# Performance work log

Measured on AMD Instinct MI355X. Metric: run time of the kernel, lower is better.

The kernel has to match this reference:

```python
import jax, jax.numpy as jnp
import numpy as np

NG, K, LEN_KEEP = 128, 32, 32  # n_groups, group_size, int(128*(1-0.75))
ENC_HEADS, DEC_HEADS = 12, 16


def _fps(xyz, init, npoint):
    # iterative farthest point sampling; xyz (B,N,3), init (B,) start indices
    B, N, _ = xyz.shape
    def step(carry, _):
        dmin, far = carry
        c = jnp.take_along_axis(xyz, far[:, None, None], axis=1)  # (B,1,3)
        dmin = jnp.minimum(dmin, jnp.sum((xyz - c) ** 2, -1))
        return (dmin, jnp.argmax(dmin, -1)), far
    _, cents = jax.lax.scan(step, (jnp.full((B, N), 1e10, xyz.dtype), init), None, length=npoint)
    return cents.T  # (B, npoint)


def _knn(xyz, cents, k):
    # squared-distance knn (same ordering as euclidean cdist + topk smallest)
    x2 = jnp.sum(xyz * xyz, -1)          # (B,N)
    c2 = jnp.sum(cents * cents, -1)      # (B,M)
    d = c2[:, :, None] + x2[:, None, :] - 2.0 * jnp.einsum('bmc,bnc->bmn', cents, xyz)
    idx = jax.lax.top_k(-d, k)[1]        # (B,M,k)
    return jax.vmap(lambda p, i: p[i])(xyz, idx)  # (B,M,k,3)


def _bn(x, g, b):
    # train-mode BatchNorm1d over (batch, spatial), channel-last x (BM,k,C)
    m = x.mean((0, 1))
    v = x.var((0, 1))
    return (x - m) * jax.lax.rsqrt(v + 1e-5) * g + b


def _ln(x, g, b):
    m = x.mean(-1, keepdims=True)
    v = ((x - m) ** 2).mean(-1, keepdims=True)
    return (x - m) * jax.lax.rsqrt(v + 1e-5) * g + b


def _layer(x, qw, qb, ow, ob, l1g, l1b, f1w, f1b, f2w, f2b, l2g, l2b, nh):
    # post-norm TransformerEncoderLayer (relu FFN, no dropout = eval mode)
    B, S, D = x.shape
    dh = D // nh
    q, k, v = jnp.split(x @ qw.T + qb, 3, axis=-1)
    q = q.reshape(B, S, nh, dh); k = k.reshape(B, S, nh, dh); v = v.reshape(B, S, nh, dh)
    att = jax.nn.softmax(jnp.einsum('bqhd,bkhd->bhqk', q, k) * (1.0 / float(np.sqrt(dh))), axis=-1)
    o = jnp.einsum('bhqk,bkhd->bqhd', att, v).reshape(B, S, D) @ ow.T + ob
    x = _ln(x + o, l1g, l1b)
    f = jax.nn.relu(x @ f1w.T + f1b) @ f2w.T + f2b
    return _ln(x + f, l2g, l2b)


def _stack(x, qw, qb, ow, ob, l1g, l1b, f1w, f1b, f2w, f2b, l2g, l2b, nh):
    for i in range(qw.shape[0]):
        x = _layer(x, qw[i], qb[i], ow[i], ob[i], l1g[i], l1b[i], f1w[i], f1b[i], f2w[i], f2b[i], l2g[i], l2b[i], nh)
    return x


def _forward(xyz, fps_init, ids_shuffle, cw1, cb1, g1, be1, cw2, cb2, g2, be2, cw3, cb3, g3, be3, pos_w, pos_b, eqw, eqb, eow, eob, el1g, el1b, ef1w, ef1b, ef2w, ef2b, el2g, el2b, dew, deb, mtok, dpw, dpb, dqw, dqb, dow, dob, dl1g, dl1b, df1w, df1b, df2w, df2b, dl2g, dl2b, prw, prb):
    B = xyz.shape[0]
    cent_idx = _fps(xyz, fps_init, NG)
    cxyz = jax.vmap(lambda p, i: p[i])(xyz, cent_idx)      # (B,NG,3)
    gn = _knn(xyz, cxyz, K) - cxyz[:, :, None, :]          # (B,NG,K,3) centered groups
    h = gn.reshape(-1, K, 3)
    h = jax.nn.relu(_bn(h @ cw1.T + cb1, g1, be1))
    h = jax.nn.relu(_bn(h @ cw2.T + cb2, g2, be2))
    h = _bn(h @ cw3.T + cb3, g3, be3)
    tokens = h.max(axis=1).reshape(B, NG, -1)              # (B,NG,768)
    x = tokens + cxyz @ pos_w.T + pos_b
    ids_restore = jnp.argsort(ids_shuffle, axis=1)
    xk = jnp.take_along_axis(x, ids_shuffle[:, :LEN_KEEP, None], axis=1)
    mask = jnp.ones((B, NG), xyz.dtype).at[:, :LEN_KEEP].set(0.0)
    mask = jnp.take_along_axis(mask, ids_restore, axis=1)
    lat = _stack(xk, eqw, eqb, eow, eob, el1g, el1b, ef1w, ef1b, ef2w, ef2b, el2g, el2b, ENC_HEADS)
    y = lat @ dew.T + deb
    mt = jnp.broadcast_to(mtok, (B, NG - LEN_KEEP, mtok.shape[0]))
    y_ = jnp.take_along_axis(jnp.concatenate([y, mt], axis=1), ids_restore[:, :, None], axis=1)
    yd = y_ + cxyz @ dpw.T + dpb
    dec = _stack(yd, dqw, dqb, dow, dob, dl1g, dl1b, df1w, df1b, df2w, df2b, dl2g, dl2b, DEC_HEADS)
    pred = dec @ prw.T + prb                               # (B,NG,K*3)
    target = gn.reshape(B, NG, -1)                         # same FPS seed -> same centroids in loss branch
    l = ((pred - target) ** 2).mean(-1)
    loss = (l * mask).sum() / mask.sum()
    return loss, pred, mask


def setup_inputs():
    ks = iter(jax.random.split(jax.random.key(0), 64))
    def W(*shape):
        return jax.random.normal(next(ks), shape, jnp.float32) * 0.02
    B, N, D, DD, Le, Ld = 32, 8192, 768, 512, 12, 8
    d = {}
    d['xyz'] = jax.random.normal(next(ks), (B, N, 3), jnp.float32)
    d['fps_init'] = jax.random.randint(next(ks), (B,), 0, N)
    d['ids_shuffle'] = jnp.argsort(jax.random.uniform(next(ks), (B, NG)), axis=1)
    d['cw1'], d['cb1'], d['g1'], d['be1'] = W(64, 3), jnp.zeros(64), jnp.ones(64), jnp.zeros(64)
    d['cw2'], d['cb2'], d['g2'], d['be2'] = W(128, 64), jnp.zeros(128), jnp.ones(128), jnp.zeros(128)
    d['cw3'], d['cb3'], d['g3'], d['be3'] = W(D, 128), jnp.zeros(D), jnp.ones(D), jnp.zeros(D)
    d['pos_w'], d['pos_b'] = W(D, 3), jnp.zeros(D)
    d['eqw'], d['eqb'] = W(Le, 3 * D, D), jnp.zeros((Le, 3 * D))
    d['eow'], d['eob'] = W(Le, D, D), jnp.zeros((Le, D))
    d['el1g'], d['el1b'] = jnp.ones((Le, D)), jnp.zeros((Le, D))
    d['ef1w'], d['ef1b'] = W(Le, 4 * D, D), jnp.zeros((Le, 4 * D))
    d['ef2w'], d['ef2b'] = W(Le, D, 4 * D), jnp.zeros((Le, D))
    d['el2g'], d['el2b'] = jnp.ones((Le, D)), jnp.zeros((Le, D))
    d['dew'], d['deb'] = W(DD, D), jnp.zeros(DD)
    d['mtok'] = jnp.zeros(DD)
    d['dpw'], d['dpb'] = W(DD, 3), jnp.zeros(DD)
    d['dqw'], d['dqb'] = W(Ld, 3 * DD, DD), jnp.zeros((Ld, 3 * DD))
    d['dow'], d['dob'] = W(Ld, DD, DD), jnp.zeros((Ld, DD))
    d['dl1g'], d['dl1b'] = jnp.ones((Ld, DD)), jnp.zeros((Ld, DD))
    d['df1w'], d['df1b'] = W(Ld, 4 * DD, DD), jnp.zeros((Ld, 4 * DD))
    d['df2w'], d['df2b'] = W(Ld, DD, 4 * DD), jnp.zeros((Ld, DD))
    d['dl2g'], d['dl2b'] = jnp.ones((Ld, DD)), jnp.zeros((Ld, DD))
    d['prw'], d['prb'] = W(K * 3, DD), jnp.zeros(K * 3)
    return d


def reference(xyz, fps_init, ids_shuffle, cw1, cb1, g1, be1, cw2, cb2, g2, be2, cw3, cb3, g3, be3, pos_w, pos_b, eqw, eqb, eow, eob, el1g, el1b, ef1w, ef1b, ef2w, ef2b, el2g, el2b, dew, deb, mtok, dpw, dpb, dqw, dqb, dow, dob, dl1g, dl1b, df1w, df1b, df2w, df2b, dl2g, dl2b, prw, prb):
    return _forward(xyz, fps_init, ids_shuffle, cw1, cb1, g1, be1, cw2, cb2, g2, be2, cw3, cb3, g3, be3, pos_w, pos_b, eqw, eqb, eow, eob, el1g, el1b, ef1w, ef1b, ef2w, ef2b, el2g, el2b, dew, deb, mtok, dpw, dpb, dqw, dqb, dow, dob, dl1g, dl1b, df1w, df1b, df2w, df2b, dl2g, dl2b, prw, prb)
```

## Files before the change

### kernel.cpp

```cpp
#include <hip/hip_runtime.h>
#include <cmath>

#define BB 32
#define NPTS 8192
#define NG 128
#define KNB 32
#define LK 32
#define DE 768
#define DD 512
#define NLE 12
#define NLD 8

typedef __bf16 bf16x8 __attribute__((ext_vector_type(8)));
typedef float  f32x4  __attribute__((ext_vector_type(4)));
typedef unsigned long long u64;

#define WAITV(N) asm volatile("s_waitcnt vmcnt(" #N ")" ::: "memory")

static __device__ __forceinline__ bf16x8 pack8(float4 a, float4 b) {
    bf16x8 h;
    h[0] = (__bf16)a.x; h[1] = (__bf16)a.y; h[2] = (__bf16)a.z; h[3] = (__bf16)a.w;
    h[4] = (__bf16)b.x; h[5] = (__bf16)b.y; h[6] = (__bf16)b.z; h[7] = (__bf16)b.w;
    return h;
}
// ... 41 lines not shown
        float best = -1.0f; int bi = 0;
        #pragma unroll
        for (int k = 0; k < 16; ++k) {
            int n = tid + (k << 9);
            float dx = x[k] - cx, dy = y[k] - cy, dz = z[k] - cz;
            float d = dx * dx + dy * dy + dz * dz;
            float dm = dmin[k];
            if (d < dm) dm = d;
            dmin[k] = dm;
            if (dm > best) { best = dm; bi = n; }
        }
        u64 key = ((u64)__float_as_uint(best) << 32) | (unsigned)(8191 - bi);
        #pragma unroll
        for (int d = 32; d >= 1; d >>= 1) {
            u64 k2 = __shfl_down(key, d);
            if (k2 > key) key = k2;
        }
        if ((tid & 63) == 0) red[t & 1][tid >> 6] = key;
        __syncthreads();
        u64 kb = red[t & 1][0];
        #pragma unroll
        for (int w = 1; w < 8; ++w) {
            u64 k2 = red[t & 1][w];
            if (k2 > kb) kb = k2;
        }
        far = 8191 - (int)(kb & 0xFFFFFFFFu);
    }
}

__global__ __launch_bounds__(256) void knn_kernel(
    const float* __restrict__ xyz, const float* __restrict__ cxyz,
    float* __restrict__ gn)
{
#pragma clang fp contract(off)
    const int bm = blockIdx.x;
    const int b = bm / NG;
    const float* P = xyz + (size_t)b * NPTS * 3;
    __shared__ u64 cand[512];
    __shared__ u64 tmins[4];
    __shared__ int wcnt[4];
    __shared__ int order[KNB];
    const int tid = threadIdx.x;
    const int wv = tid >> 6, lane = tid & 63;
    const float cx = cxyz[bm * 3 + 0], cy = cxyz[bm * 3 + 1], cz = cxyz[bm * 3 + 2];
    const float c2 = cx * cx + cy * cy + cz * cz;
    unsigned fk[32];
    float bestf = 1e31f; int bi = 1 << 30;
    #pragma unroll
    for (int j = 0; j < 32; ++j) {
        int n = tid + (j << 8);
        float x = P[n * 3 + 0], y = P[n * 3 + 1], z = P[n * 3 + 2];
        float x2 = x * x + y * y + z * z;
        float dt = cx * x + cy * y + cz * z;
        float v = (c2 + x2) - 2.0f * dt;
        fk[j] = fkey(v);
        if (v < bestf) { bestf = v; bi = n; }
    }
    u64 mk = ((u64)fkey(bestf) << 32) | (unsigned)bi;
    {
        u64 v = mk;
        #pragma unroll
        for (int k = 2; k <= 64; k <<= 1) {
            #pragma unroll
            for (int j = k >> 1; j > 0; j >>= 1) {
                u64 o = __shfl_xor(v, j);
                bool up = ((lane & k) == 0);
                bool lower = ((lane & j) == 0);
                u64 mn = (v < o) ? v : o;
                u64 mx = (v < o) ? o : v;
                v = (up == lower) ? mn : mx;
            }
        }
        u64 Tw = __shfl(v, 31);
        if (lane == 0) tmins[wv] = Tw;
    }
    __syncthreads();
    u64 T = tmins[0];
    #pragma unroll
    for (int w = 1; w < 4; ++w) { u64 k2 = tmins[w]; if (k2 < T) T = k2; }
    int c = 0;
    #pragma unroll
    for (int j = 0; j < 32; ++j) {
        u64 key = ((u64)fk[j] << 32) | (unsigned)(tid + (j << 8));
        c += (key <= T) ? 1 : 0;
    }
    int s = c;
    #pragma unroll
    for (int d = 1; d < 64; d <<= 1) {
        int t2 = __shfl_up(s, d);
        if (lane >= d) s += t2;
    }
    int excl = s - c;
    if (lane == 63) wcnt[wv] = s;
    __syncthreads();
    int base = 0;
    for (int w = 0; w < wv; ++w) base += wcnt[w];
    int etot = wcnt[0] + wcnt[1] + wcnt[2] + wcnt[3];

    if (etot <= 512) {
        int pos = base + excl;
        #pragma unroll
        for (int j = 0; j < 32; ++j) {
            u64 key = ((u64)fk[j] << 32) | (unsigned)(tid + (j << 8));
            if (key <= T) cand[pos++] = key;
        }
        __syncthreads();
        for (int si = tid; si < etot; si += 256) {
            u64 my = cand[si];
            int r = 0;
            for (int j2 = 0; j2 < etot; ++j2) r += (cand[j2] < my) ? 1 : 0;
            if (r < KNB) order[r] = (int)(my & 0xFFFFFFFFu);
        }
        __syncthreads();
    } else {
        u64 bk = ~0ull;
        #pragma unroll
        for (int j = 0; j < 32; ++j) {
            u64 key = ((u64)fk[j] << 32) | (unsigned)(tid + (j << 8));
            if (key < bk) bk = key;
        }
        for (int r = 0; r < KNB; ++r) {
            u64 kk = bk;
            #pragma unroll
            for (int dd = 32; dd >= 1; dd >>= 1) {
                u64 k2 = __shfl_down(kk, dd);
                if (k2 < kk) kk = k2;
            }
            if (lane == 0) cand[(r & 1) * 4 + wv] = kk;
            __syncthreads();
            u64 kb = cand[(r & 1) * 4 + 0];
            #pragma unroll
            for (int w = 1; w < 4; ++w) { u64 k2 = cand[(r & 1) * 4 + w]; if (k2 < kb) kb = k2; }
            if (tid == 0) order[r] = (int)(kb & 0xFFFFFFFFu);
            if ((int)(kb & 255u) == tid) {
                int sj = (int)((kb & 0xFFFFFFFFu) >> 8);
                #pragma unroll
                for (int j = 0; j < 32; ++j) if (j == sj) fk[j] = 0xFFFFFFFFu;
                bk = ~0ull;
                #pragma unroll
                for (int j = 0; j < 32; ++j) {
                    u64 key = ((u64)fk[j] << 32) | (unsigned)(tid + (j << 8));
                    if (key < bk) bk = key;
                }
            }
            __syncthreads();
        }
    }
    if (tid < KNB) {
        int n = order[tid];
        gn[((size_t)bm * KNB + tid) * 3 + 0] = P[n * 3 + 0] - cx;
        gn[((size_t)bm * KNB + tid) * 3 + 1] = P[n * 3 + 1] - cy;
        gn[((size_t)bm * KNB + tid) * 3 + 2] = P[n * 3 + 2] - cz;
    }
}

__global__ void cvt_bf16_kernel(const float* __restrict__ src, __bf16* __restrict__ dst, int n8)
{
    int i = blockIdx.x * 256 + threadIdx.x;
    if (i >= n8) return;
    const float4* p = (const float4*)(src + (size_t)i * 8);
    *(bf16x8*)(dst + (size_t)i * 8) = pack8(p[0], p[1]);
}

struct CvtTab {
    const float* src[10];
    __bf16* dst[10];
    int cum[11];
};
__global__ void cvt_multi_kernel(CvtTab t)
{
    int i = blockIdx.x * 256 + threadIdx.x;
    if (i >= t.cum[10]) return;
    int seg = 0;
    #pragma unroll
    for (int k = 1; k < 10; ++k) seg += (i >= t.cum[k]) ? 1 : 0;
    int local = i - t.cum[seg];
    const float4* p = (const float4*)(t.src[seg] + (size_t)local * 8);
    *(bf16x8*)(t.dst[seg] + (size_t)local * 8) = pack8(p[0], p[1]);
}

__global__ void embed1_kernel(const float* __restrict__ gn, const float* __restrict__ w,
                              const float* __restrict__ bias, float* __restrict__ h1)
{
    int i = blockIdx.x * 256 + threadIdx.x;
    if (i >= 131072 * 64) return;
    int r = i >> 6, c = i & 63;
    const float* p = gn + (size_t)r * 3;
    h1[i] = p[0] * w[c * 3 + 0] + p[1] * w[c * 3 + 1] + p[2] * w[c * 3 + 2] + bias[c];
}

template <int C>
__global__ __launch_bounds__(256) void colstats_kernel(const float* __restrict__ X,
                                                       double* __restrict__ st, int Mrows)
{
    constexpr int RL = 256 / C;
    const int c = threadIdx.x % C;
    const int rl = threadIdx.x / C;
    double s = 0.0, s2 = 0.0;
    int rows_per_block = (Mrows + gridDim.x - 1) / gridDim.x;
    int r0 = blockIdx.x * rows_per_block;
    int r1 = min(r0 + rows_per_block, Mrows);
    for (int r = r0 + rl; r < r1; r += RL) {
        float v = X[(size_t)r * C + c];
        s += v; s2 += (double)v * v;
    }
    __shared__ double sh[2][256];
    sh[0][threadIdx.x] = s; sh[1][threadIdx.x] = s2;
    __syncthreads();
    if (rl == 0) {
        for (int j = 1; j < RL; ++j) { s += sh[0][j * C + c]; s2 += sh[1][j * C + c]; }
        atomicAdd(&st[c], s);
        atomicAdd(&st[C + c], s2);
    }
}

__global__ void bn_finalize(const double* __restrict__ st, const float* __restrict__ g,
                            const float* __restrict__ be, float* __restrict__ sc,
                            float* __restrict__ shb, int C)
{
    int c = blockIdx.x * 64 + threadIdx.x;
    if (c >= C) return;
    double m = st[c] / 131072.0;
    double var = st[C + c] / 131072.0 - m * m;
    if (var < 0.0) var = 0.0;
    float rs = rsqrtf((float)var + 1e-5f);
    sc[c] = rs * g[c];
    shb[c] = be[c] - (float)m * rs * g[c];
}

__global__ void bn_apply_bf16(const float* __restrict__ x, const float* __restrict__ sc,
                              const float* __restrict__ shb, __bf16* __restrict__ y,
                              int total, int C)
{
    int i = blockIdx.x * 256 + threadIdx.x;
    if (i >= total) return;
    int c = i % C;
    float v = x[i] * sc[c] + shb[c];
    v = fmaxf(v, 0.0f);
    y[i] = (__bf16)v;
}

template <int BM, int WM, int WN, int DEPTH>
__global__ __launch_bounds__(256) void gemm_bf16(
    const __bf16* __restrict__ A, const __bf16* __restrict__ W,
    const float* __restrict__ bias, float* __restrict__ Cf, __bf16* __restrict__ Cb,
    int M, int N, int K, int Kc, int relu)
{
    constexpr int MR = BM / WM / 16;
    constexpr int NR = 128 / WN / 16;
    constexpr int CA = BM * 8 / 256;
    __shared__ __bf16 As[DEPTH][BM * 64];
    __shared__ __bf16 Ws[DEPTH][128 * 64];
    const int tid = threadIdx.x;
    const int lane = tid & 63;
    const int wave = tid >> 6;
    const int wm = wave / WN, wn = wave % WN;
    const int m0 = blockIdx.y * BM, n0 = blockIdx.x * 128;
    const int kb = blockIdx.z * Kc;

    f32x4 acc[MR][NR] = {};

    auto stage = [&](int buf, int kt) {
        #pragma unroll
        for (int j = 0; j < CA; ++j) {
            int cb = j * 256 + (wave << 6);
            int c  = cb + lane;
            int row = c >> 3;
            int kcs = (c & 7) ^ (row & 7);
            gload16(A + (size_t)(m0 + row) * K + kb + kt + kcs * 8, &As[buf][cb * 8]);
        }
        #pragma unroll
        for (int j = 0; j < 4; ++j) {
            int cb = j * 256 + (wave << 6);
            int c  = cb + lane;
            int row = c >> 3;
            int kcs = (c & 7) ^ (row & 7);
            gload16(W + (size_t)(n0 + row) * K + kb + kt + kcs * 8, &Ws[buf][cb * 8]);
        }
    };
    auto compute = [&](int buf) {
        #pragma unroll
        for (int ks = 0; ks < 2; ++ks) {
            bf16x8 af[MR], bfr[NR];
            int kc = ks * 4 + (lane >> 4);
            #pragma unroll
            for (int i = 0; i < MR; ++i) {
                int rowA = wm * (BM / WM) + i * 16 + (lane & 15);
                af[i] = *(bf16x8*)&As[buf][rowA * 64 + ((kc ^ (rowA & 7)) * 8)];
            }
            #pragma unroll
            for (int j = 0; j < NR; ++j) {
                int rowB = wn * (128 / WN) + j * 16 + (lane & 15);
                bfr[j] = *(bf16x8*)&Ws[buf][rowB * 64 + ((kc ^ (rowB & 7)) * 8)];
            }
            #pragma unroll
            for (int i = 0; i < MR; ++i)
                #pragma unroll
                for (int j = 0; j < NR; ++j)
                    acc[i][j] = __builtin_amdgcn_mfma_f32_16x16x32_bf16(af[i], bfr[j], acc[i][j], 0, 0, 0);
        }
    };

    const int nt = Kc >> 6;
    if constexpr (DEPTH == 3) {
        stage(0, 0);
        if (nt > 1) stage(1, 64);
        for (int t = 0; t < nt; ++t) {
            if (t < nt - 1) { if constexpr (BM == 64) WAITV(6); else WAITV(8); }
            else            WAITV(0);
            __syncthreads();
            if (t + 2 < nt) stage((t + 2) % 3, (t + 2) << 6);
            compute(t % 3);
        }
    } else {
        stage(0, 0);
        if (nt > 1) stage(1, 64);
        for (int t = 0; t < nt; ++t) {
            if (t < nt - 1) { if constexpr (BM == 64) WAITV(6); else WAITV(8); }
            else            WAITV(0);
            __syncthreads();
            compute(t % 2);
            if (t + 2 <= nt - 1) {
                __syncthreads();
                stage(t % 2, (t + 2) << 6);
            }
        }
    }

    float* Co = Cf ? Cf + (size_t)blockIdx.z * M * N : nullptr;
    #pragma unroll
    for (int j = 0; j < NR; ++j) {
        int col = n0 + wn * (128 / WN) + j * 16 + (lane & 15);
        if (col >= N) continue;
        float bv = (blockIdx.z == 0) ? bias[col] : 0.0f;
        #pragma unroll
        for (int i = 0; i < MR; ++i) {
            #pragma unroll
            for (int r = 0; r < 4; ++r) {
                int rowm = m0 + wm * (BM / WM) + i * 16 + (lane >> 4) * 4 + r;
                float v = acc[i][j][r] + bv;
                if (relu) v = fmaxf(v, 0.0f);
                if (Co) Co[(size_t)rowm * N + col] = v;
                if (Cb) Cb[(size_t)rowm * N + col] = (__bf16)v;
            }
        }
    }
}

__global__ __launch_bounds__(256) void embed3_mfma(
    const __bf16* __restrict__ A, const __bf16* __restrict__ W,
    const float* __restrict__ cb3,
    float* __restrict__ gmax, float* __restrict__ gmin, double* __restrict__ st3)
{
    __shared__ __bf16 As[2][128 * 64];
    __shared__ __bf16 Ws[2][128 * 64];
    const int tid = threadIdx.x;
    const int lane = tid & 63;
    const int wave = tid >> 6;
    const int wm = wave >> 1, wn = wave & 1;
    const int m0 = blockIdx.y * 128, n0 = blockIdx.x * 128;
    const int K = 128;

    f32x4 acc[4][4] = {};

    auto stage = [&](int buf, int kt) {
        #pragma unroll
        for (int j = 0; j < 4; ++j) {
            int cb = j * 256 + (wave << 6);
            int c  = cb + lane;
            int row = c >> 3;
            int kcs = (c & 7) ^ (row & 7);
            gload16(A + (size_t)(m0 + row) * K + kt + kcs * 8, &As[buf][cb * 8]);
            gload16(W + (size_t)(n0 + row) * K + kt + kcs * 8, &Ws[buf][cb * 8]);
        }
    };
    auto compute = [&](int buf) {
        #pragma unroll
        for (int ks = 0; ks < 2; ++ks) {
            bf16x8 af[4], bfr[4];
            int kc = ks * 4 + (lane >> 4);
            #pragma unroll
            for (int i = 0; i < 4; ++i) {
                int rowA = wm * 64 + i * 16 + (lane & 15);
                af[i] = *(bf16x8*)&As[buf][rowA * 64 + ((kc ^ (rowA & 7)) * 8)];
                int rowB = wn * 64 + i * 16 + (lane & 15);
                bfr[i] = *(bf16x8*)&Ws[buf][rowB * 64 + ((kc ^ (rowB & 7)) * 8)];
            }
            #pragma unroll
            for (int i = 0; i < 4; ++i)
                #pragma unroll
                for (int j = 0; j < 4; ++j)
                    acc[i][j] = __builtin_amdgcn_mfma_f32_16x16x32_bf16(af[i], bfr[j], acc[i][j], 0, 0, 0);
        }
    };

    stage(0, 0);
    stage(1, 64);
    WAITV(8);
    __syncthreads();
    compute(0);
    WAITV(0);
    __syncthreads();
    compute(1);

    #pragma unroll
    for (int j = 0; j < 4; ++j) {
        int col = n0 + wn * 64 + j * 16 + (lane & 15);
        float bv = cb3[col];
        float stot = 0.0f, s2tot = 0.0f;
        #pragma unroll
        for (int gi = 0; gi < 2; ++gi) {
            float mx = -1e30f, mn = 1e30f, s = 0.0f, s2 = 0.0f;
            #pragma unroll
            for (int ii = 0; ii < 2; ++ii) {
                f32x4 a = acc[gi * 2 + ii][j];
                #pragma unroll
                for (int r = 0; r < 4; ++r) {
                    float v = a[r] + bv;
                    mx = fmaxf(mx, v); mn = fminf(mn, v);
                    s += v; s2 += v * v;
                }
            }
            #pragma unroll
            for (int d = 16; d < 64; d <<= 1) {
                mx = fmaxf(mx, __shfl_xor(mx, d));
                mn = fminf(mn, __shfl_xor(mn, d));
                s  += __shfl_xor(s, d);
                s2 += __shfl_xor(s2, d);
            }
            stot += s; s2tot += s2;
            if (lane < 16) {
                int g = (m0 >> 5) + wm * 2 + gi;
                gmax[(size_t)g * 768 + col] = mx;
                gmin[(size_t)g * 768 + col] = mn;
            }
        }
        if (lane < 16) {
            double* stp = st3 + (size_t)(blockIdx.y & 31) * 1536;
            atomicAdd(&stp[col], (double)stot);
            atomicAdd(&stp[768 + col], (double)s2tot);
        }
    }
}

__global__ void bn3_finalize(const double* __restrict__ st3, const float* __restrict__ g,
                             const float* __restrict__ be, float* __restrict__ a3,
                             float* __restrict__ c3)
{
    int c = blockIdx.x * 256 + threadIdx.x;
    if (c >= 768) return;
    double s = 0.0, s2 = 0.0;
    for (int p = 0; p < 32; ++p) { s += st3[(size_t)p * 1536 + c]; s2 += st3[(size_t)p * 1536 + 768 + c]; }
    double m = s / 131072.0;
    double var = s2 / 131072.0 - m * m;
    if (var < 0.0) var = 0.0;
    float rs = rsqrtf((float)var + 1e-5f);
    a3[c] = rs * g[c];
    c3[c] = be[c] - (float)m * rs * g[c];
}

__global__ void tokens_pos(const float* __restrict__ gmax, const float* __restrict__ gmin,
                           const float* __restrict__ a3, const float* __restrict__ c3,
                           const float* __restrict__ cxyz, const float* __restrict__ posw,
                           const float* __restrict__ posb, float* __restrict__ x)
{
    int i = blockIdx.x * 256 + threadIdx.x;
    if (i >= 4096 * 768) return;
    int c = i % 768, g = i / 768;
    float a = a3[c];
    float tok = (a >= 0.0f ? a * gmax[i] : a * gmin[i]) + c3[c];
    float px = cxyz[g * 3 + 0], py = cxyz[g * 3 + 1], pz = cxyz[g * 3 + 2];
    x[i] = tok + px * posw[c * 3 + 0] + py * posw[c * 3 + 1] + pz * posw[c * 3 + 2] + posb[c];
}

__global__ void restore_kernel(const int* __restrict__ shuffle, int* __restrict__ restore,
                               float* __restrict__ maskv)
{
    int j = blockIdx.x * 256 + threadIdx.x;
    if (j >= BB * NG) return;
    int b = j / NG, p = j % NG;
    int dst = b * NG + shuffle[j];
    restore[dst] = p;
    maskv[dst] = (p < LK) ? 0.0f : 1.0f;
}

__global__ void gather_xk(const float* __restrict__ xfull, const int* __restrict__ shuffle,
                          float* __restrict__ xe, __bf16* __restrict__ xeb)
{
    int i = blockIdx.x * 256 + threadIdx.x;
    if (i >= BB * LK * DE) return;
    int c = i % DE;
    int s = (i / DE) % LK;
    int b = i / (DE * LK);
    float v = xfull[((size_t)b * NG + shuffle[b * NG + s]) * DE + c];
    xe[i] = v;
    xeb[i] = (__bf16)v;
}

__global__ void yd_build(const float* __restrict__ ykp, const int* __restrict__ restore,
                         const float* __restrict__ mtok, const float* __restrict__ cxyz,
                         const float* __restrict__ dpw, const float* __restrict__ dpb,
                         float* __restrict__ xd, __bf16* __restrict__ xdb)
{
    const size_t PS = (size_t)1024 * DD;
    int i = blockIdx.x * 256 + threadIdx.x;
    if (i >= BB * NG * DD) return;
    int c = i % DD;
    int g = i / DD;
    int b = g / NG;
    int r = restore[g];
    float base;
    if (r < LK) {
        size_t o = (size_t)(b * LK + r) * DD + c;
        base = ykp[o] + ykp[PS + o] + ykp[2 * PS + o] + ykp[3 * PS + o];
    } else {
        base = mtok[c];
    }
    float px = cxyz[g * 3 + 0], py = cxyz[g * 3 + 1], pz = cxyz[g * 3 + 2];
    float v = base + px * dpw[c * 3 + 0] + py * dpw[c * 3 + 1] + pz * dpw[c * 3 + 2] + dpb[c];
    xd[i] = v;
    xdb[i] = (__bf16)v;
}

template <int S, int DH, int NH>
__global__ __launch_bounds__(256) void dattn_kernel(const float* __restrict__ qkv,
                                                    __bf16* __restrict__ o, float scale)
{
    constexpr int D = NH * DH;
    constexpr int SQ = DH + 8;
    constexpr int SV = S + 8;
    __shared__ __bf16 Qb[S * SQ];
    __shared__ __bf16 Kb[S * SQ];
    __shared__ __bf16 Vt[DH * SV];
    __shared__ __bf16 Pb[S * SV];
    const int h = blockIdx.x % NH;
    const int b = blockIdx.x / NH;
    const int tid = threadIdx.x;
    const int lane = tid & 63, wv = tid >> 6;
    const float* base = qkv + (size_t)b * S * 3 * D + h * DH;
    for (int i = tid; i < S * (DH / 4); i += 256) {
        int s = i / (DH / 4), c4 = (i % (DH / 4)) * 4;
        const float* rp = base + (size_t)s * 3 * D;
        float4 q = *(const float4*)(rp + c4);
        float4 k = *(const float4*)(rp + D + c4);
        float4 v = *(const float4*)(rp + 2 * D + c4);
        __bf16 q4[4] = {(__bf16)q.x, (__bf16)q.y, (__bf16)q.z, (__bf16)q.w};
        __bf16 k4[4] = {(__bf16)k.x, (__bf16)k.y, (__bf16)k.z, (__bf16)k.w};
        *(ushort4*)&Qb[s * SQ + c4] = *(ushort4*)q4;
        *(ushort4*)&Kb[s * SQ + c4] = *(ushort4*)k4;
        Vt[(c4 + 0) * SV + s] = (__bf16)v.x;
        Vt[(c4 + 1) * SV + s] = (__bf16)v.y;
        Vt[(c4 + 2) * SV + s] = (__bf16)v.z;
        Vt[(c4 + 3) * SV + s] = (__bf16)v.w;
    }
    __syncthreads();
    const int q0 = wv * 32;
    const int arow = lane & 15;
    const int kch = (lane >> 4) * 8;
    const int rrow = (lane >> 4) * 4;
    f32x4 sc[2][8];
    {
        bf16x8 af0 = *(bf16x8*)&Qb[(q0 + arow) * SQ + kch];
        bf16x8 af1 = *(bf16x8*)&Qb[(q0 + 16 + arow) * SQ + kch];
        f32x4 z = {0.0f, 0.0f, 0.0f, 0.0f};
        #pragma unroll
        for (int j = 0; j < 8; ++j) {
            bf16x8 bf_ = *(bf16x8*)&Kb[(j * 16 + arow) * SQ + kch];
            sc[0][j] = __builtin_amdgcn_mfma_f32_16x16x32_bf16(af0, bf_, z, 0, 0, 0);
            sc[1][j] = __builtin_amdgcn_mfma_f32_16x16x32_bf16(af1, bf_, z, 0, 0, 0);
        }
    }
    #pragma unroll
    for (int i = 0; i < 2; ++i) {
        #pragma unroll
        for (int r = 0; r < 4; ++r) {
            float m = -1e30f;
            #pragma unroll
            for (int j = 0; j < 8; ++j) m = fmaxf(m, sc[i][j][r]);
            #pragma unroll
            for (int d = 8; d >= 1; d >>= 1) m = fmaxf(m, __shfl_xor(m, d));
            float sum = 0.0f;
            #pragma unroll
            for (int j = 0; j < 8; ++j) {
                float e = expf((sc[i][j][r] - m) * scale);
                sc[i][j][r] = e;
                sum += e;
            }
            #pragma unroll
            for (int d = 8; d >= 1; d >>= 1) sum += __shfl_xor(sum, d);
            float inv = 1.0f / sum;
            int row = q0 + i * 16 + rrow + r;
            #pragma unroll
            for (int j = 0; j < 8; ++j)
                Pb[row * SV + j * 16 + (lane & 15)] = (__bf16)(sc[i][j][r] * inv);
        }
    }
    #pragma unroll
    for (int i = 0; i < 2; ++i) {
        #pragma unroll
        for (int j2 = 0; j2 < 2; ++j2) {
            f32x4 a2 = {0.0f, 0.0f, 0.0f, 0.0f};
            #pragma unroll
            for (int ks = 0; ks < 4; ++ks) {
                bf16x8 pa = *(bf16x8*)&Pb[(q0 + i * 16 + arow) * SV + ks * 32 + kch];
                bf16x8 vb = *(bf16x8*)&Vt[(j2 * 16 + arow) * SV + ks * 32 + kch];
                a2 = __builtin_amdgcn_mfma_f32_16x16x32_bf16(pa, vb, a2, 0, 0, 0);
            }
            #pragma unroll
            for (int r = 0; r < 4; ++r) {
                int q = q0 + i * 16 + rrow + r;
                o[((size_t)(b * S + q)) * D + h * DH + j2 * 16 + (lane & 15)] = (__bf16)a2[r];
            }
        }
    }
}

template <int S, int DH, int NH>
__global__ __launch_bounds__(64) void eattn_kernel(const float* __restrict__ qkv,
                                                   __bf16* __restrict__ o, float scale)
{
    constexpr int D = NH * DH;
    constexpr int SQ = DH + 8;
    constexpr int SV = S + 8;
    __shared__ __bf16 Qb[S * SQ];
    __shared__ __bf16 Kb[S * SQ];
    __shared__ __bf16 Vt[DH * SV];
    __shared__ __bf16 Pb[S * SV];
    const int h = blockIdx.x % NH;
    const int b = blockIdx.x / NH;
    const int lane = threadIdx.x;
    const float* base = qkv + (size_t)b * S * 3 * D + h * DH;
    for (int i = lane; i < S * (DH / 4); i += 64) {
        int s = i / (DH / 4), c4 = (i % (DH / 4)) * 4;
        const float* rp = base + (size_t)s * 3 * D;
        float4 q = *(const float4*)(rp + c4);
        float4 k = *(const float4*)(rp + D + c4);
        float4 v = *(const float4*)(rp + 2 * D + c4);
        __bf16 q4[4] = {(__bf16)q.x, (__bf16)q.y, (__bf16)q.z, (__bf16)q.w};
        __bf16 k4[4] = {(__bf16)k.x, (__bf16)k.y, (__bf16)k.z, (__bf16)k.w};
        *(ushort4*)&Qb[s * SQ + c4] = *(ushort4*)q4;
        *(ushort4*)&Kb[s * SQ + c4] = *(ushort4*)k4;
        Vt[(c4 + 0) * SV + s] = (__bf16)v.x;
        Vt[(c4 + 1) * SV + s] = (__bf16)v.y;
        Vt[(c4 + 2) * SV + s] = (__bf16)v.z;
        Vt[(c4 + 3) * SV + s] = (__bf16)v.w;
    }
    __syncthreads();
    const int arow = lane & 15;
    const int kch = (lane >> 4) * 8;
    const int rrow = (lane >> 4) * 4;
    f32x4 sc[2][2] = {};
    #pragma unroll
    for (int ks = 0; ks < 2; ++ks) {
        bf16x8 af0 = *(bf16x8*)&Qb[(arow) * SQ + ks * 32 + kch];
        bf16x8 af1 = *(bf16x8*)&Qb[(16 + arow) * SQ + ks * 32 + kch];
        #pragma unroll
        for (int j = 0; j < 2; ++j) {
            bf16x8 bf_ = *(bf16x8*)&Kb[(j * 16 + arow) * SQ + ks * 32 + kch];
            sc[0][j] = __builtin_amdgcn_mfma_f32_16x16x32_bf16(af0, bf_, sc[0][j], 0, 0, 0);
            sc[1][j] = __builtin_amdgcn_mfma_f32_16x16x32_bf16(af1, bf_, sc[1][j], 0, 0, 0);
        }
    }
    #pragma unroll
    for (int i = 0; i < 2; ++i) {
        #pragma unroll
        for (int r = 0; r < 4; ++r) {
            float m = fmaxf(sc[i][0][r], sc[i][1][r]);
            #pragma unroll
            for (int d = 8; d >= 1; d >>= 1) m = fmaxf(m, __shfl_xor(m, d));
            float sum = 0.0f;
            #pragma unroll
            for (int j = 0; j < 2; ++j) {
                float e = expf((sc[i][j][r] - m) * scale);
                sc[i][j][r] = e;
                sum += e;
            }
            #pragma unroll
            for (int d = 8; d >= 1; d >>= 1) sum += __shfl_xor(sum, d);
            float inv = 1.0f / sum;
            int row = i * 16 + rrow + r;
            #pragma unroll
            for (int j = 0; j < 2; ++j)
                Pb[row * SV + j * 16 + (lane & 15)] = (__bf16)(sc[i][j][r] * inv);
        }
    }
    __syncthreads();
    #pragma unroll
    for (int i = 0; i < 2; ++i) {
        bf16x8 pa = *(bf16x8*)&Pb[(i * 16 + arow) * SV + kch];
        #pragma unroll
        for (int j2 = 0; j2 < 4; ++j2) {
            bf16x8 vb = *(bf16x8*)&Vt[(j2 * 16 + arow) * SV + kch];
            f32x4 z = {0.0f, 0.0f, 0.0f, 0.0f};
            f32x4 a2 = __builtin_amdgcn_mfma_f32_16x16x32_bf16(pa, vb, z, 0, 0, 0);
            #pragma unroll
            for (int r = 0; r < 4; ++r) {
                int q = i * 16 + rrow + r;
                o[((size_t)(b * S + q)) * D + h * DH + j2 * 16 + (lane & 15)] = (__bf16)a2[r];
            }
        }
    }
}

template <int D, int SK>
__global__ __launch_bounds__(256) void ln_res(float* __restrict__ x, const float* __restrict__ part,
                                              size_t pstride,
                                              const float* __restrict__ g, const float* __restrict__ b,
                                              __bf16* __restrict__ xb)
{
    constexpr int J = D / 256;
    __shared__ float pr[2][4];
    const size_t off = (size_t)blockIdx.x * D;
    const int tid = threadIdx.x;
    float vals[J];
    float s = 0.0f, s2 = 0.0f;
    #pragma unroll
    for (int j = 0; j < J; ++j) {
        int i = tid + j * 256;
        float v = x[off + i];
        #pragma unroll
        for (int sk = 0; sk < SK; ++sk) v += part[(size_t)sk * pstride + off + i];
        vals[j] = v; s += v; s2 += v * v;
    }
    #pragma unroll
    for (int d = 32; d >= 1; d >>= 1) { s += __shfl_down(s, d); s2 += __shfl_down(s2, d); }
    if ((tid & 63) == 0) { pr[0][tid >> 6] = s; pr[1][tid >> 6] = s2; }
    __syncthreads();
    float st = pr[0][0] + pr[0][1] + pr[0][2] + pr[0][3];
    float s2t = pr[1][0] + pr[1][1] + pr[1][2] + pr[1][3];
    float m = st / D;
    float var = s2t / D - m * m;
    if (var < 0.0f) var = 0.0f;
    float rs = rsqrtf(var + 1e-5f);
    #pragma unroll
    for (int j = 0; j < J; ++j) {
        int i = tid + j * 256;
        float v = (vals[j] - m) * rs * g[i] + b[i];
        x[off + i] = v;
        xb[off + i] = (__bf16)v;
    }
}

__global__ __launch_bounds__(128) void loss_l(const float* __restrict__ pred,
                                              const float* __restrict__ target,
                                              const float* __restrict__ maskv,
                                              float* __restrict__ lm)
{
    const int g = blockIdx.x;
    __shared__ float red[128];
    int t = threadIdx.x;
    float s = 0.0f;
    if (t < 96) {
        float d = pred[(size_t)g * 96 + t] - target[(size_t)g * 96 + t];
        s = d * d;
    }
    red[t] = s; __syncthreads();
    for (int st = 64; st > 0; st >>= 1) { if (t < st) red[t] += red[t + st]; __syncthreads(); }
    if (t == 0) lm[g] = (red[0] / 96.0f) * maskv[g];
}

__global__ __launch_bounds__(1024) void loss_final(const float* __restrict__ lm,
                                                   const float* __restrict__ maskv,
                                                   float* __restrict__ out)
{
    __shared__ float r1[1024], r2[1024];
    int t = threadIdx.x;
    float a = 0.0f, b = 0.0f;
    for (int i = t; i < BB * NG; i += 1024) { a += lm[i]; b += maskv[i]; }
    r1[t] = a; r2[t] = b; __syncthreads();
    for (int st = 512; st > 0; st >>= 1) { if (t < st) { r1[t] += r1[t + st]; r2[t] += r2[t + st]; } __syncthreads(); }
    if (t == 0) out[0] = r1[0] / r2[0];
}

extern "C" void kernel_launch(void* const* d_in, const int* in_sizes, int n_in,
                              void* d_out, int out_size, void* d_ws, size_t ws_size,
                              hipStream_t stream)
{
    (void)in_sizes; (void)n_in; (void)out_size; (void)ws_size;
    const float* xyz        = (const float*)d_in[0];
    const int*   fps_init   = (const int*)d_in[1];
    const int*   ids_shuf   = (const int*)d_in[2];
    const float* cw1 = (const float*)d_in[3];  const float* cb1 = (const float*)d_in[4];
    const float* g1  = (const float*)d_in[5];  const float* be1 = (const float*)d_in[6];
    const float* cw2 = (const float*)d_in[7];  const float* cb2 = (const float*)d_in[8];
    const float* g2  = (const float*)d_in[9];  const float* be2 = (const float*)d_in[10];
    const float* cw3 = (const float*)d_in[11]; const float* cb3 = (const float*)d_in[12];
    const float* g3  = (const float*)d_in[13]; const float* be3 = (const float*)d_in[14];
    const float* posw = (const float*)d_in[15]; const float* posb = (const float*)d_in[16];
    const float* eqw = (const float*)d_in[17]; const float* eqb = (const float*)d_in[18];
    const float* eow = (const float*)d_in[19]; const float* eob = (const float*)d_in[20];
    const float* el1g = (const float*)d_in[21]; const float* el1b = (const float*)d_in[22];
    const float* ef1w = (const float*)d_in[23]; const float* ef1b = (const float*)d_in[24];
    const float* ef2w = (const float*)d_in[25]; const float* ef2b = (const float*)d_in[26];
    const float* el2g = (const float*)d_in[27]; const float* el2b = (const float*)d_in[28];
    const float* dew = (const float*)d_in[29]; const float* deb = (const float*)d_in[30];
    const float* mtok = (const float*)d_in[31];
    const float* dpw = (const float*)d_in[32]; const float* dpb = (const float*)d_in[33];
    const float* dqw = (const float*)d_in[34]; const float* dqb = (const float*)d_in[35];
    const float* dow = (const float*)d_in[36]; const float* dob = (const float*)d_in[37];
    const float* dl1g = (const float*)d_in[38]; const float* dl1b = (const float*)d_in[39];
    const float* df1w = (const float*)d_in[40]; const float* df1b = (const float*)d_in[41];
    const float* df2w = (const float*)d_in[42]; const float* df2b = (const float*)d_in[43];
    const float* dl2g = (const float*)d_in[44]; const float* dl2b = (const float*)d_in[45];
    const float* prw = (const float*)d_in[46]; const float* prb = (const float*)d_in[47];
    float* out = (float*)d_out;
    float* pred = out + 1;
    float* maskv = out + 1 + (size_t)BB * NG * KNB * 3;

    char* ws = (char*)d_ws;
    size_t off = 0;
    auto alloc = [&](size_t bytes) -> void* {
        void* p = ws + off;
        off = (off + bytes + 255) & ~(size_t)255;
        return p;
    };
    double* st1 = (double*)alloc(128 * 8);
    double* st2 = (double*)alloc(256 * 8);
    double* st3 = (double*)alloc((size_t)32 * 1536 * 8);
    float* sc1 = (float*)alloc(64 * 4);  float* sh1 = (float*)alloc(64 * 4);
    float* sc2 = (float*)alloc(128 * 4); float* sh2 = (float*)alloc(128 * 4);
    float* a3 = (float*)alloc(768 * 4);  float* c3 = (float*)alloc(768 * 4);
    int* restore = (int*)alloc(4096 * 4);
    float* cxyz = (float*)alloc(12288 * 4);
    float* gn   = (float*)alloc((size_t)393216 * 4);
    __bf16* cw2b = (__bf16*)alloc((size_t)128 * 64 * 2);
    __bf16* cw3b = (__bf16*)alloc((size_t)768 * 128 * 2);
    float* xfull = (float*)alloc((size_t)4096 * 768 * 4);
    float* xe    = (float*)alloc((size_t)1024 * 768 * 4);
    __bf16* xeb  = (__bf16*)alloc((size_t)1024 * 768 * 2);
    float* qkve  = (float*)alloc((size_t)1024 * 2304 * 4);
    __bf16* oeb  = (__bf16*)alloc((size_t)1024 * 768 * 2);
    __bf16* fe1b = (__bf16*)alloc((size_t)1024 * 3072 * 2);
    float* xd    = (float*)alloc((size_t)4096 * 512 * 4);
    __bf16* xdb  = (__bf16*)alloc((size_t)4096 * 512 * 2);
    float* qkvd  = (float*)alloc((size_t)4096 * 1536 * 4);
    __bf16* odb  = (__bf16*)alloc((size_t)4096 * 512 * 2);
    __bf16* fd1b = (__bf16*)alloc((size_t)4096 * 2048 * 2);
    float* lm    = (float*)alloc(4096 * 4);

    __bf16* eqwb  = (__bf16*)alloc((size_t)NLE * 3 * DE * DE * 2);
    __bf16* eowb  = (__bf16*)alloc((size_t)NLE * DE * DE * 2);
    __bf16* ef1wb = (__bf16*)alloc((size_t)NLE * 4 * DE * DE * 2);
    __bf16* ef2wb = (__bf16*)alloc((size_t)NLE * 4 * DE * DE * 2);
    __bf16* dewb  = (__bf16*)alloc((size_t)DD * DE * 2);
    __bf16* dqwb  = (__bf16*)alloc((size_t)NLD * 3 * DD * DD * 2);
    __bf16* dowb  = (__bf16*)alloc((size_t)NLD * DD * DD * 2);
    __bf16* df1wb = (__bf16*)alloc((size_t)NLD * 4 * DD * DD * 2);
    __bf16* df2wb = (__bf16*)alloc((size_t)NLD * 4 * DD * DD * 2);
    __bf16* prwb  = (__bf16*)alloc((size_t)128 * 512 * 2);

    char* U = (char*)eqwb;
    float*  h1   = (float*)U;
    __bf16* h1b  = (__bf16*)(U + (size_t)33554432);
    float*  h2   = (float*)(U + (size_t)50331648);
    __bf16* h2b  = (__bf16*)(U + (size_t)117440512);
    float*  gmax = (float*)(U + (size_t)150994944);
    float*  gmin = (float*)(U + (size_t)163577856);

    size_t stats_bytes = (size_t)((char*)st3 + (size_t)32 * 1536 * 8 - (char*)st1);
    hipMemsetAsync((void*)st1, 0, stats_bytes, stream);

    auto cvt = [&](const float* src, __bf16* dst, size_t n) {
        int n8 = (int)(n / 8);
        cvt_bf16_kernel<<<(n8 + 255) / 256, 256, 0, stream>>>(src, dst, n8);
    };
    auto gemm = [&](const __bf16* A, const __bf16* Wt, const float* bias,
                    float* Cf, __bf16* Cb, int M, int N, int K, int relu) {
        int nb128 = ((N + 127) / 128) * (M / 128);
        if (nb128 < 256) {
            dim3 grid((N + 127) / 128, M / 64, 1);
            gemm_bf16<64, 1, 4, 3><<<grid, 256, 0, stream>>>(A, Wt, bias, Cf, Cb, M, N, K, K, relu);
        } else {
            dim3 grid((N + 127) / 128, M / 128, 1);
            gemm_bf16<128, 2, 2, 2><<<grid, 256, 0, stream>>>(A, Wt, bias, Cf, Cb, M, N, K, K, relu);
        }
    };
    auto gemmSK = [&](const __bf16* A, const __bf16* Wt, const float* bias,
                      float* Cf, int M, int N, int K, int SK) {
        dim3 grid((N + 127) / 128, M / 64, SK);
        gemm_bf16<64, 1, 4, 3><<<grid, 256, 0, stream>>>(A, Wt, bias, Cf, nullptr, M, N, K, K / SK, 0);
    };

    cvt(cw2, cw2b, 128 * 64);
    cvt(cw3, cw3b, 768 * 128);

    fps_kernel<<<BB, 512, 0, stream>>>(xyz, fps_init, cxyz);
    knn_kernel<<<BB * NG, 256, 0, stream>>>(xyz, cxyz, gn);

    embed1_kernel<<<(131072 * 64 + 255) / 256, 256, 0, stream>>>(gn, cw1, cb1, h1);
    colstats_kernel<64><<<256, 256, 0, stream>>>(h1, st1, 131072);
    bn_finalize<<<1, 64, 0, stream>>>(st1, g1, be1, sc1, sh1, 64);
    bn_apply_bf16<<<(131072 * 64 + 255) / 256, 256, 0, stream>>>(h1, sc1, sh1, h1b, 131072 * 64, 64);
    gemm(h1b, cw2b, cb2, h2, nullptr, 131072, 128, 64, 0);
    colstats_kernel<128><<<256, 256, 0, stream>>>(h2, st2, 131072);
    bn_finalize<<<2, 64, 0, stream>>>(st2, g2, be2, sc2, sh2, 128);
    bn_apply_bf16<<<(131072 * 128 + 255) / 256, 256, 0, stream>>>(h2, sc2, sh2, h2b, 131072 * 128, 128);
    embed3_mfma<<<dim3(6, 1024), 256, 0, stream>>>(h2b, cw3b, cb3, gmax, gmin, st3);
    bn3_finalize<<<3, 256, 0, stream>>>(st3, g3, be3, a3, c3);
    tokens_pos<<<(4096 * 768 + 255) / 256, 256, 0, stream>>>(gmax, gmin, a3, c3, cxyz, posw, posb, xfull);

    restore_kernel<<<16, 256, 0, stream>>>(ids_shuf, restore, maskv);
    gather_xk<<<(BB * LK * DE + 255) / 256, 256, 0, stream>>>(xfull, ids_shuf, xe, xeb);

    {
        CvtTab t;
        const float* srcs[10] = {eqw, eow, ef1w, ef2w, dew, dqw, dow, df1w, df2w, prw};
        __bf16* dsts[10] = {eqwb, eowb, ef1wb, ef2wb, dewb, dqwb, dowb, df1wb, df2wb, prwb};
        size_t ns[10] = {
            (size_t)NLE * 3 * DE * DE, (size_t)NLE * DE * DE,
            (size_t)NLE * 4 * DE * DE, (size_t)NLE * 4 * DE * DE,
            (size_t)DD * DE,
            (size_t)NLD * 3 * DD * DD, (size_t)NLD * DD * DD,
            (size_t)NLD * 4 * DD * DD, (size_t)NLD * 4 * DD * DD,
            (size_t)96 * 512
        };
        int cum = 0;
        t.cum[0] = 0;
        for (int k = 0; k < 10; ++k) {
            t.src[k] = srcs[k]; t.dst[k] = dsts[k];
            cum += (int)(ns[k] / 8);
            t.cum[k + 1] = cum;
        }
        cvt_multi_kernel<<<(cum + 255) / 256, 256, 0, stream>>>(t);
        hipMemsetAsync((void*)(prwb + (size_t)96 * 512), 0, (size_t)32 * 512 * 2, stream);
    }

    const size_t PSE = (size_t)1024 * DE;
    const size_t PSD = (size_t)4096 * DD;

    for (int l = 0; l < NLE; ++l) {
        gemm(xeb, eqwb + (size_t)l * 3 * DE * DE, eqb + (size_t)l * 3 * DE, qkve, nullptr, 1024, 3 * DE, DE, 0);
        eattn_kernel<LK, 64, 12><<<BB * 12, 64, 0, stream>>>(qkve, oeb, 0.125f);
        gemmSK(oeb, eowb + (size_t)l * DE * DE, eob + (size_t)l * DE, xfull, 1024, DE, DE, 4);
        ln_res<DE, 4><<<BB * LK, 256, 0, stream>>>(xe, xfull, PSE, el1g + (size_t)l * DE, el1b + (size_t)l * DE, xeb);
        gemm(xeb, ef1wb + (size_t)l * 4 * DE * DE, ef1b + (size_t)l * 4 * DE, nullptr, fe1b, 1024, 4 * DE, DE, 1);
        gemmSK(fe1b, ef2wb + (size_t)l * DE * 4 * DE, ef2b + (size_t)l * DE, xfull, 1024, DE, 4 * DE, 4);
        ln_res<DE, 4><<<BB * LK, 256, 0, stream>>>(xe, xfull, PSE, el2g + (size_t)l * DE, el2b + (size_t)l * DE, xeb);
    }

    gemmSK(xeb, dewb, deb, qkve, 1024, DD, DE, 4);
    yd_build<<<(BB * NG * DD + 255) / 256, 256, 0, stream>>>(qkve, restore, mtok, cxyz, dpw, dpb, xd, xdb);

    const float dsc = (float)(1.0 / sqrt(32.0));
    for (int l = 0; l < NLD; ++l) {
        gemm(xdb, dqwb + (size_t)l * 3 * DD * DD, dqb + (size_t)l * 3 * DD, qkvd, nullptr, 4096, 3 * DD, DD, 0);
        dattn_kernel<NG, 32, 16><<<BB * 16, 256, 0, stream>>>(qkvd, odb, dsc);
        gemmSK(odb, dowb + (size_t)l * DD * DD, dob + (size_t)l * DD, qkvd, 4096, DD, DD, 2);
        ln_res<DD, 2><<<BB * NG, 256, 0, stream>>>(xd, qkvd, PSD, dl1g + (size_t)l * DD, dl1b + (size_t)l * DD, xdb);
        gemm(xdb, df1wb + (size_t)l * 4 * DD * DD, df1b + (size_t)l * 4 * DD, nullptr, fd1b, 4096, 4 * DD, DD, 1);
        gemmSK(fd1b, df2wb + (size_t)l * DD * 4 * DD, df2b + (size_t)l * DD, qkvd, 4096, DD, 4 * DD, 2);
        ln_res<DD, 2><<<BB * NG, 256, 0, stream>>>(xd, qkvd, PSD, dl2g + (size_t)l * DD, dl2b + (size_t)l * DD, xdb);
    }

    gemm(xdb, prwb, prb, pred, nullptr, 4096, 96, 512, 0);
    loss_l<<<BB * NG, 128, 0, stream>>>(pred, gn, maskv, lm);
    loss_final<<<1, 1024, 0, stream>>>(lm, maskv, out);
}
```

Before: 2.419 ms.

## Store QKV in bf16, fuse token gather into tokens_pos, split-K prediction head

The QKV projections now write bf16 instead of fp32, and both attention kernels load bf16x8 vectors directly, which halves QKV traffic and drops the in-kernel conversion. tokens_pos now writes only the kept tokens straight into the encoder input via the restore map, which removes the full xfull write and the separate gather kernel. The final projection uses split-K with the partial sums reduced inside loss_l. The GEMM pipeline loop is unified across depths, and gmax/gmin/predp reuse existing buffers. Risks are reduced precision in QKV and aliasing errors if the reused buffers are still live when overwritten.

```diff
diff --git a/kernel.cpp b/kernel.cpp
--- a/kernel.cpp
+++ b/kernel.cpp
@@ -367,29 +367,15 @@
     };
 
     const int nt = Kc >> 6;
-    if constexpr (DEPTH == 3) {
-        stage(0, 0);
-        if (nt > 1) stage(1, 64);
-        for (int t = 0; t < nt; ++t) {
-            if (t < nt - 1) { if constexpr (BM == 64) WAITV(6); else WAITV(8); }
-            else            WAITV(0);
-            __syncthreads();
-            if (t + 2 < nt) stage((t + 2) % 3, (t + 2) << 6);
-            compute(t % 3);
-        }
-    } else {
-        stage(0, 0);
-        if (nt > 1) stage(1, 64);
-        for (int t = 0; t < nt; ++t) {
-            if (t < nt - 1) { if constexpr (BM == 64) WAITV(6); else WAITV(8); }
-            else            WAITV(0);
-            __syncthreads();
-            compute(t % 2);
-            if (t + 2 <= nt - 1) {
-                __syncthreads();
-                stage(t % 2, (t + 2) << 6);
-            }
-        }
+    stage(0, 0);
+    if (DEPTH > 2 && nt > 1) stage(1, 64);
+    for (int t = 0; t < nt; ++t) {
+        int ahead = min(nt - 1, t + DEPTH - 2) - t;
+        if (ahead >= 1) { if constexpr (BM == 64) WAITV(6); else WAITV(8); }
+        else            WAITV(0);
+        __syncthreads();
+        if (t + DEPTH - 1 < nt) stage((t + DEPTH - 1) % DEPTH, (t + DEPTH - 1) << 6);
+        compute(t % DEPTH);
     }
 
     float* Co = Cf ? Cf + (size_t)blockIdx.z * M * N : nullptr;
@@ -527,15 +513,22 @@
 __global__ void tokens_pos(const float* __restrict__ gmax, const float* __restrict__ gmin,
                            const float* __restrict__ a3, const float* __restrict__ c3,
                            const float* __restrict__ cxyz, const float* __restrict__ posw,
-                           const float* __restrict__ posb, float* __restrict__ x)
+                           const float* __restrict__ posb, const int* __restrict__ restore,
+                           float* __restrict__ xe, __bf16* __restrict__ xeb)
 {
     int i = blockIdx.x * 256 + threadIdx.x;
     if (i >= 4096 * 768) return;
     int c = i % 768, g = i / 768;
+    int r = restore[g];
+    if (r >= LK) return;
     float a = a3[c];
     float tok = (a >= 0.0f ? a * gmax[i] : a * gmin[i]) + c3[c];
     float px = cxyz[g * 3 + 0], py = cxyz[g * 3 + 1], pz = cxyz[g * 3 + 2];
-    x[i] = tok + px * posw[c * 3 + 0] + py * posw[c * 3 + 1] + pz * posw[c * 3 + 2] + posb[c];
+    float v = tok + px * posw[c * 3 + 0] + py * posw[c * 3 + 1] + pz * posw[c * 3 + 2] + posb[c];
+    int b = g >> 7;
+    size_t idx = ((size_t)(b * LK + r)) * DE + c;
+    xe[idx] = v;
+    xeb[idx] = (__bf16)v;
 }
 
 __global__ void restore_kernel(const int* __restrict__ shuffle, int* __restrict__ restore,
@@ -547,19 +540,6 @@
     int dst = b * NG + shuffle[j];
     restore[dst] = p;
     maskv[dst] = (p < LK) ? 0.0f : 1.0f;
-}
-
-__global__ void gather_xk(const float* __restrict__ xfull, const int* __restrict__ shuffle,
-                          float* __restrict__ xe, __bf16* __restrict__ xeb)
-{
-    int i = blockIdx.x * 256 + threadIdx.x;
-    if (i >= BB * LK * DE) return;
-    int c = i % DE;
-    int s = (i / DE) % LK;
-    int b = i / (DE * LK);
-    float v = xfull[((size_t)b * NG + shuffle[b * NG + s]) * DE + c];
-    xe[i] = v;
-    xeb[i] = (__bf16)v;
 }
 
 __global__ void yd_build(const float* __restrict__ ykp, const int* __restrict__ restore,
@@ -588,7 +568,7 @@
 }
 
 template <int S, int DH, int NH>
-__global__ __launch_bounds__(256) void dattn_kernel(const float* __restrict__ qkv,
+__global__ __launch_bounds__(256) void dattn_kernel(const __bf16* __restrict__ qkv,
                                                     __bf16* __restrict__ o, float scale)
 {
     constexpr int D = NH * DH;
@@ -602,21 +582,17 @@
     const int b = blockIdx.x / NH;
     const int tid = threadIdx.x;
     const int lane = tid & 63, wv = tid >> 6;
-    const float* base = qkv + (size_t)b * S * 3 * D + h * DH;
-    for (int i = tid; i < S * (DH / 4); i += 256) {
-        int s = i / (DH / 4), c4 = (i % (DH / 4)) * 4;
-        const float* rp = base + (size_t)s * 3 * D;
-        float4 q = *(const float4*)(rp + c4);
-        float4 k = *(const float4*)(rp + D + c4);
-        float4 v = *(const float4*)(rp + 2 * D + c4);
-        __bf16 q4[4] = {(__bf16)q.x, (__bf16)q.y, (__bf16)q.z, (__bf16)q.w};
-        __bf16 k4[4] = {(__bf16)k.x, (__bf16)k.y, (__bf16)k.z, (__bf16)k.w};
-        *(ushort4*)&Qb[s * SQ + c4] = *(ushort4*)q4;
-        *(ushort4*)&Kb[s * SQ + c4] = *(ushort4*)k4;
-        Vt[(c4 + 0) * SV + s] = (__bf16)v.x;
-        Vt[(c4 + 1) * SV + s] = (__bf16)v.y;
-        Vt[(c4 + 2) * SV + s] = (__bf16)v.z;
-        Vt[(c4 + 3) * SV + s] = (__bf16)v.w;
+    const __bf16* base = qkv + (size_t)b * S * 3 * D + h * DH;
+    for (int i = tid; i < S * (DH / 8); i += 256) {
+        int s = i / (DH / 8), c8 = (i % (DH / 8)) * 8;
+        const __bf16* rp = base + (size_t)s * 3 * D;
+        bf16x8 q = *(const bf16x8*)(rp + c8);
+        bf16x8 k = *(const bf16x8*)(rp + D + c8);
+        bf16x8 v = *(const bf16x8*)(rp + 2 * D + c8);
+        *(bf16x8*)&Qb[s * SQ + c8] = q;
+        *(bf16x8*)&Kb[s * SQ + c8] = k;
+        #pragma unroll
+        for (int j = 0; j < 8; ++j) Vt[(c8 + j) * SV + s] = v[j];
     }
     __syncthreads();
     const int q0 = wv * 32;
@@ -681,7 +657,7 @@
 }
 
 template <int S, int DH, int NH>
-__global__ __launch_bounds__(64) void eattn_kernel(const float* __restrict__ qkv,
+__global__ __launch_bounds__(64) void eattn_kernel(const __bf16* __restrict__ qkv,
                                                    __bf16* __restrict__ o, float scale)
 {
     constexpr int D = NH * DH;
@@ -694,21 +670,17 @@
     const int h = blockIdx.x % NH;
     const int b = blockIdx.x / NH;
     const int lane = threadIdx.x;
-    const float* base = qkv + (size_t)b * S * 3 * D + h * DH;
-    for (int i = lane; i < S * (DH / 4); i += 64) {
-        int s = i / (DH / 4), c4 = (i % (DH / 4)) * 4;
-        const float* rp = base + (size_t)s * 3 * D;
-        float4 q = *(const float4*)(rp + c4);
-        float4 k = *(const float4*)(rp + D + c4);
-        float4 v = *(const float4*)(rp + 2 * D + c4);
-        __bf16 q4[4] = {(__bf16)q.x, (__bf16)q.y, (__bf16)q.z, (__bf16)q.w};
-        __bf16 k4[4] = {(__bf16)k.x, (__bf16)k.y, (__bf16)k.z, (__bf16)k.w};
-        *(ushort4*)&Qb[s * SQ + c4] = *(ushort4*)q4;
-        *(ushort4*)&Kb[s * SQ + c4] = *(ushort4*)k4;
-        Vt[(c4 + 0) * SV + s] = (__bf16)v.x;
-        Vt[(c4 + 1) * SV + s] = (__bf16)v.y;
-        Vt[(c4 + 2) * SV + s] = (__bf16)v.z;
-        Vt[(c4 + 3) * SV + s] = (__bf16)v.w;
+    const __bf16* base = qkv + (size_t)b * S * 3 * D + h * DH;
+    for (int i = lane; i < S * (DH / 8); i += 64) {
+        int s = i / (DH / 8), c8 = (i % (DH / 8)) * 8;
+        const __bf16* rp = base + (size_t)s * 3 * D;
+        bf16x8 q = *(const bf16x8*)(rp + c8);
+        bf16x8 k = *(const bf16x8*)(rp + D + c8);
+        bf16x8 v = *(const bf16x8*)(rp + 2 * D + c8);
+        *(bf16x8*)&Qb[s * SQ + c8] = q;
+        *(bf16x8*)&Kb[s * SQ + c8] = k;
+        #pragma unroll
+        for (int j = 0; j < 8; ++j) Vt[(c8 + j) * SV + s] = v[j];
     }
     __syncthreads();
     const int arow = lane & 15;
@@ -806,17 +778,22 @@
     }
 }
 
-__global__ __launch_bounds__(128) void loss_l(const float* __restrict__ pred,
+__global__ __launch_bounds__(128) void loss_l(const float* __restrict__ predp,
                                               const float* __restrict__ target,
                                               const float* __restrict__ maskv,
+                                              float* __restrict__ pred_out,
                                               float* __restrict__ lm)
 {
+    const size_t PS = (size_t)4096 * 96;
     const int g = blockIdx.x;
     __shared__ float red[128];
     int t = threadIdx.x;
     float s = 0.0f;
     if (t < 96) {
-        float d = pred[(size_t)g * 96 + t] - target[(size_t)g * 96 + t];
+        size_t o = (size_t)g * 96 + t;
+        float v = predp[o] + predp[PS + o] + predp[2 * PS + o] + predp[3 * PS + o];
+        pred_out[o] = v;
+        float d = v - target[o];
         s = d * d;
     }
     red[t] = s; __syncthreads();
@@ -894,11 +871,13 @@
     float* xe    = (float*)alloc((size_t)1024 * 768 * 4);
     __bf16* xeb  = (__bf16*)alloc((size_t)1024 * 768 * 2);
     float* qkve  = (float*)alloc((size_t)1024 * 2304 * 4);
+    __bf16* qkveb = (__bf16*)alloc((size_t)1024 * 2304 * 2);
     __bf16* oeb  = (__bf16*)alloc((size_t)1024 * 768 * 2);
     __bf16* fe1b = (__bf16*)alloc((size_t)1024 * 3072 * 2);
     float* xd    = (float*)alloc((size_t)4096 * 512 * 4);
     __bf16* xdb  = (__bf16*)alloc((size_t)4096 * 512 * 2);
     float* qkvd  = (float*)alloc((size_t)4096 * 1536 * 4);
+    __bf16* qkvdb = (__bf16*)alloc((size_t)4096 * 1536 * 2);
     __bf16* odb  = (__bf16*)alloc((size_t)4096 * 512 * 2);
     __bf16* fd1b = (__bf16*)alloc((size_t)4096 * 2048 * 2);
     float* lm    = (float*)alloc(4096 * 4);
@@ -919,8 +898,9 @@
     __bf16* h1b  = (__bf16*)(U + (size_t)33554432);
     float*  h2   = (float*)(U + (size_t)50331648);
     __bf16* h2b  = (__bf16*)(U + (size_t)117440512);
-    float*  gmax = (float*)(U + (size_t)150994944);
-    float*  gmin = (float*)(U + (size_t)163577856);
+    float* gmax = qkvd;
+    float* gmin = qkvd + (size_t)3145728;
+    float* predp = (float*)fd1b;
 
     size_t stats_bytes = (size_t)((char*)st3 + (size_t)32 * 1536 * 8 - (char*)st1);
     hipMemsetAsync((void*)st1, 0, stats_bytes, stream);
@@ -962,10 +942,10 @@
     bn_apply_bf16<<<(131072 * 128 + 255) / 256, 256, 0, stream>>>(h2, sc2, sh2, h2b, 131072 * 128, 128);
     embed3_mfma<<<dim3(6, 1024), 256, 0, stream>>>(h2b, cw3b, cb3, gmax, gmin, st3);
     bn3_finalize<<<3, 256, 0, stream>>>(st3, g3, be3, a3, c3);
-    tokens_pos<<<(4096 * 768 + 255) / 256, 256, 0, stream>>>(gmax, gmin, a3, c3, cxyz, posw, posb, xfull);
 
     restore_kernel<<<16, 256, 0, stream>>>(ids_shuf, restore, maskv);
-    gather_xk<<<(BB * LK * DE + 255) / 256, 256, 0, stream>>>(xfull, ids_shuf, xe, xeb);
+    tokens_pos<<<(4096 * 768 + 255) / 256, 256, 0, stream>>>(gmax, gmin, a3, c3, cxyz, posw, posb,
+                                                             restore, xe, xeb);
 
     {
         CvtTab t;
@@ -994,8 +974,8 @@
     const size_t PSD = (size_t)4096 * DD;
 
     for (int l = 0; l < NLE; ++l) {
-        gemm(xeb, eqwb + (size_t)l * 3 * DE * DE, eqb + (size_t)l * 3 * DE, qkve, nullptr, 1024, 3 * DE, DE, 0);
-        eattn_kernel<LK, 64, 12><<<BB * 12, 64, 0, stream>>>(qkve, oeb, 0.125f);
+        gemm(xeb, eqwb + (size_t)l * 3 * DE * DE, eqb + (size_t)l * 3 * DE, nullptr, qkveb, 1024, 3 * DE, DE, 0);
+        eattn_kernel<LK, 64, 12><<<BB * 12, 64, 0, stream>>>(qkveb, oeb, 0.125f);
         gemmSK(oeb, eowb + (size_t)l * DE * DE, eob + (size_t)l * DE, xfull, 1024, DE, DE, 4);
         ln_res<DE, 4><<<BB * LK, 256, 0, stream>>>(xe, xfull, PSE, el1g + (size_t)l * DE, el1b + (size_t)l * DE, xeb);
         gemm(xeb, ef1wb + (size_t)l * 4 * DE * DE, ef1b + (size_t)l * 4 * DE, nullptr, fe1b, 1024, 4 * DE, DE, 1);
@@ -1008,8 +988,8 @@
 
     const float dsc = (float)(1.0 / sqrt(32.0));
     for (int l = 0; l < NLD; ++l) {
-        gemm(xdb, dqwb + (size_t)l * 3 * DD * DD, dqb + (size_t)l * 3 * DD, qkvd, nullptr, 4096, 3 * DD, DD, 0);
-        dattn_kernel<NG, 32, 16><<<BB * 16, 256, 0, stream>>>(qkvd, odb, dsc);
+        gemm(xdb, dqwb + (size_t)l * 3 * DD * DD, dqb + (size_t)l * 3 * DD, nullptr, qkvdb, 4096, 3 * DD, DD, 0);
+        dattn_kernel<NG, 32, 16><<<BB * 16, 256, 0, stream>>>(qkvdb, odb, dsc);
         gemmSK(odb, dowb + (size_t)l * DD * DD, dob + (size_t)l * DD, qkvd, 4096, DD, DD, 2);
         ln_res<DD, 2><<<BB * NG, 256, 0, stream>>>(xd, qkvd, PSD, dl1g + (size_t)l * DD, dl1b + (size_t)l * DD, xdb);
         gemm(xdb, df1wb + (size_t)l * 4 * DD * DD, df1b + (size_t)l * 4 * DD, nullptr, fd1b, 4096, 4 * DD, DD, 1);
@@ -1017,7 +997,7 @@
         ln_res<DD, 2><<<BB * NG, 256, 0, stream>>>(xd, qkvd, PSD, dl2g + (size_t)l * DD, dl2b + (size_t)l * DD, xdb);
     }
 
-    gemm(xdb, prwb, prb, pred, nullptr, 4096, 96, 512, 0);
-    loss_l<<<BB * NG, 128, 0, stream>>>(pred, gn, maskv, lm);
+    gemmSK(xdb, prwb, prb, predp, 4096, 96, 512, 4);
+    loss_l<<<BB * NG, 128, 0, stream>>>(predp, gn, maskv, pred, lm);
     loss_final<<<1, 1024, 0, stream>>>(lm, maskv, out);
 }
```

Measured after the change: 2.376 ms. About the same (-1.8%).
